# Performance work log

Measured on AMD Instinct MI355X. Metric: run time of the kernel, lower is better.

The kernel has to match this reference:

```python
import jax, jax.numpy as jnp
import numpy as np

BN_EPS = 1e-5

def binary_activation(x):
    # ReActNet BinaryActivation: forward = sign(x), backward = piecewise poly STE
    out_fwd = jnp.sign(x)
    m1 = (x < -1.0).astype(x.dtype)
    m2 = (x < 0.0).astype(x.dtype)
    m3 = (x < 1.0).astype(x.dtype)
    out1 = -1.0 * m1 + (x * x + 2.0 * x) * (1.0 - m1)
    out2 = out1 * m2 + (-x * x + 2.0 * x) * (1.0 - m2)
    out3 = out2 * m3 + 1.0 * (1.0 - m3)
    return jax.lax.stop_gradient(out_fwd - out3) + out3

def binary_conv3x3(x, w, stride=1):
    # per-output-channel scaling = mean |w| over (in, kh, kw), detached
    scale = jax.lax.stop_gradient(jnp.mean(jnp.abs(w), axis=(1, 2, 3), keepdims=True))
    bw_no_grad = jax.lax.stop_gradient(scale * jnp.sign(w))
    cw = jnp.clip(w, -1.0, 1.0)
    bw = bw_no_grad - jax.lax.stop_gradient(cw) + cw
    return jax.lax.conv_general_dilated(
        x, bw, window_strides=(stride, stride), padding=[(1, 1), (1, 1)],
        dimension_numbers=('NCHW', 'OIHW', 'NCHW'))

def batchnorm_inference(y, gamma, beta, mean, var):
    inv = gamma * jax.lax.rsqrt(var + BN_EPS)
    return y * inv[None, :, None, None] + (beta - mean * inv)[None, :, None, None]

def setup_inputs() -> dict:
    key = jax.random.key(0)
    k1, k2, k3 = jax.random.split(key, 3)
    N, Cin, Cout, H, W = 64, 128, 128, 56, 56
    x = jax.random.normal(k1, (N, Cin, H, W), dtype=jnp.float32)
    weight = jax.random.normal(k2, (Cout, Cin, 3, 3), dtype=jnp.float32) * 0.1
    gamma = jnp.ones((Cout,), dtype=jnp.float32)
    beta = jnp.zeros((Cout,), dtype=jnp.float32)
    bn_mean = jnp.zeros((Cout,), dtype=jnp.float32)
    bn_var = jax.random.uniform(k3, (Cout,), dtype=jnp.float32)
    return {"x": x, "weight": weight, "gamma": gamma, "beta": beta,
            "bn_mean": bn_mean, "bn_var": bn_var}

def reference(x, weight, gamma, beta, bn_mean, bn_var):
    residual = x
    out = binary_activation(x)
    out = binary_conv3x3(out, weight, stride=1)
    out = batchnorm_inference(out, gamma, beta, bn_mean, bn_var)
    return out + residual
```

## Files before the change

### kernel.cpp

```cpp
#include <hip/hip_runtime.h>


#define N_   64
#define C_   128
#define H_   56
#define W_   56
#define HW_  (H_*W_)
#define PH_  (H_+2)
#define PW_  (W_+2)
#define PHW_ (PH_*PW_)
#define NPIX (N_*HW_)
#define NPAD (N_*PHW_)

typedef unsigned long long u64;

__global__ void prep_w_kernel(const float* __restrict__ w,
                              const float* __restrict__ gamma,
                              const float* __restrict__ beta,
                              const float* __restrict__ bn_mean,
                              const float* __restrict__ bn_var,
                              u64* __restrict__ wbits,
                              float* __restrict__ A, float* __restrict__ B) {
    const int o = blockIdx.x;
    const int lane = threadIdx.x;
    const float* wo = w + o * 1152;

    float s = 0.f;
    #pragma unroll
    for (int k = 0; k < 18; k++) s += fabsf(wo[k * 64 + lane]);
    #pragma unroll
    for (int off = 32; off > 0; off >>= 1) s += __shfl_down(s, off);
    float scale = __shfl(s, 0) * (1.0f / 1152.0f);

    #pragma unroll
    for (int t = 0; t < 9; t++) {
        #pragma unroll
        for (int j = 0; j < 2; j++) {
            float v = wo[(j * 64 + lane) * 9 + t];
            u64 b = __ballot(v < 0.0f);
            if (lane == 0) wbits[(o * 9 + t) * 2 + j] = b;
        }
    }
    if (lane == 0) {
        float inv = gamma[o] * rsqrtf(bn_var[o] + 1e-5f);
        A[o] = scale * inv;
        B[o] = beta[o] - bn_mean[o] * inv;
    }
}

__global__ __launch_bounds__(256) void pack_x_kernel(
        const float* __restrict__ x,
        ulonglong2* __restrict__ xbs,
        ulonglong2* __restrict__ xbz,
        unsigned* __restrict__ xcnt) {
    int t = blockIdx.x * 256 + threadIdx.x;
    int p = t * 2;
    int n = p / HW_;
    int r = p - n * HW_;
    int h = r / W_;
    int w = r - h * W_;

    const float2* xp = (const float2*)(x + (size_t)n * C_ * HW_ + h * W_ + w);

    unsigned pa[4], za[4], pb[4], zb[4];
    #pragma unroll
    for (int j = 0; j < 4; j++) { pa[j]=0; za[j]=0; pb[j]=0; zb[j]=0; }

    #pragma unroll
    for (int j = 0; j < 4; j++) {
        unsigned paj = 0, zaj = 0, pbj = 0, zbj = 0;
        #pragma unroll 16
        for (int c = 0; c < 32; c++) {
            float2 v = xp[(size_t)(j * 32 + c) * (HW_ / 2)];
            unsigned ua = __float_as_uint(v.x);
            unsigned ub = __float_as_uint(v.y);
            paj |= (ua >> 31) << c;
            zaj |= ((ua << 1) != 0u ? 1u : 0u) << c;
            pbj |= (ub >> 31) << c;
            zbj |= ((ub << 1) != 0u ? 1u : 0u) << c;
        }
        pa[j]=paj; za[j]=zaj; pb[j]=pbj; zb[j]=zbj;
    }

    int pg = (n * PH_ + h + 1) * PW_ + (w + 1);
    ulonglong2 s2, z2;
    s2.x = (u64)pa[0] | ((u64)pa[1] << 32);
    s2.y = (u64)pa[2] | ((u64)pa[3] << 32);
    z2.x = (u64)za[0] | ((u64)za[1] << 32);
    z2.y = (u64)za[2] | ((u64)za[3] << 32);
    xbs[pg] = s2; xbz[pg] = z2;
    xcnt[pg] = __popc(za[0]) + __popc(za[1]) + __popc(za[2]) + __popc(za[3]);

    s2.x = (u64)pb[0] | ((u64)pb[1] << 32);
    s2.y = (u64)pb[2] | ((u64)pb[3] << 32);
    z2.x = (u64)zb[0] | ((u64)zb[1] << 32);
    z2.y = (u64)zb[2] | ((u64)zb[3] << 32);
    xbs[pg + 1] = s2; xbz[pg + 1] = z2;
    xcnt[pg + 1] = __popc(zb[0]) + __popc(zb[1]) + __popc(zb[2]) + __popc(zb[3]);
}

__global__ void border_kernel(ulonglong2* __restrict__ xbs,
                              ulonglong2* __restrict__ xbz,
                              unsigned* __restrict__ xcnt) {
    int bt = blockIdx.x * 256 + threadIdx.x;
    if (bt >= N_ * 228) return;
    int n = bt / 228, e = bt - n * 228;
    int ph, pw;
    if (e < 58)       { ph = 0;  pw = e; }
    else if (e < 116) { ph = 57; pw = e - 58; }
    else { int i = e - 116; ph = 1 + (i >> 1); pw = (i & 1) ? 57 : 0; }
    int g = (n * PH_ + ph) * PW_ + pw;
    ulonglong2 zz; zz.x = 0; zz.y = 0;
    xbs[g] = zz; xbz[g] = zz; xcnt[g] = 0;
}

__device__ __forceinline__ int tapmask_of(int idx) {
    int tm = 0;
    if (idx & 1) tm |= 0x007;
    if (idx & 2) tm |= 0x1C0;
    if (idx & 4) tm |= 0x049;
    if (idx & 8) tm |= 0x124;
    return tm;
}

__global__ __launch_bounds__(256, 6) void bconv_kernel(
        const ulonglong2* __restrict__ xbs,
        const ulonglong2* __restrict__ xbz,
        const unsigned*   __restrict__ xcnt,
        const u64* __restrict__ wbits,
        const float* __restrict__ Ag, const float* __restrict__ Bg,
        const float* __restrict__ x, float* __restrict__ out) {
    __shared__ float2 AB_s[16 * 64];

    const int tid = threadIdx.x;
    const int obase = blockIdx.y * 64;

    for (int e = tid; e < 1024; e += 256) {
        int idx = e >> 6, o = (e & 63);
        int tm = tapmask_of(idx);
        const u64* wp = wbits + (size_t)(obase + o) * 18;
        int s = 0;
        #pragma unroll
        for (int t = 0; t < 9; t++) {
            if ((tm >> t) & 1)
                s += 128 - 2 * (__popcll(wp[2*t]) + __popcll(wp[2*t+1]));
        }
        float a = Ag[obase + o];
        float2 ab; ab.x = a; ab.y = Bg[obase + o] - a * (float)s;
        AB_s[e] = ab;
    }
    __syncthreads();

    int g = blockIdx.x * 256 + tid;
    int n = g / HW_;
    int r = g - n * HW_;
    int h = r / W_;
    int w = r - h * W_;
    int pb = (n * PH_ + h + 1) * PW_ + (w + 1);

    u64 sx[9], sy[9];
    int taps_off[9];
    int csum = 0;
    #pragma unroll
    for (int dh = 0; dh < 3; dh++) {
        #pragma unroll
        for (int dw = 0; dw < 3; dw++) {
            int k = dh * 3 + dw;
            int idx = pb + (dh - 1) * PW_ + (dw - 1);
            taps_off[k] = idx;
            ulonglong2 t2 = xbs[idx];
            sx[k] = t2.x; sy[k] = t2.y;
            csum += (int)xcnt[idx];
        }
    }

    int pidx = (h == 0 ? 1 : 0) | (h == H_-1 ? 2 : 0) |
               (w == 0 ? 4 : 0) | (w == W_-1 ? 8 : 0);
    int valid = 9 - __popc(tapmask_of(pidx));
    bool slow = (csum != 128 * valid);

    const float* xr = x   + ((size_t)n * C_ + obase) * HW_ + r;
    float*       op = out + ((size_t)n * C_ + obase) * HW_ + r;
    const float2* abp = &AB_s[pidx << 6];

    if (!slow) {
        const u64* wp = wbits + (size_t)obase * 18;
        #pragma unroll 2
        for (int o = 0; o < 64; o++) {
            int pc = 0;
            #pragma unroll
            for (int k = 0; k < 9; k++) {
                pc += __popcll(sx[k] ^ wp[2*k]);
                pc += __popcll(sy[k] ^ wp[2*k+1]);
            }
            wp += 18;
            float2 ab = abp[o];
            float dot = (float)(1152 - 2 * pc);
            op[o * HW_] = fmaf(ab.x, dot, ab.y) + xr[o * HW_];
        }
    } else {
        for (int o = 0; o < 64; o++) {
            const u64* wp = wbits + (size_t)(obase + o) * 18;
            int pc = 0;
            #pragma unroll
            for (int k = 0; k < 9; k++) {
                ulonglong2 zz = xbz[taps_off[k]];
                pc += __popcll((sx[k] ^ wp[2*k])   & zz.x);
                pc += __popcll((sy[k] ^ wp[2*k+1]) & zz.y);
            }
            float a = abp[o].x;
            int dot = csum - 2 * pc;
            op[o * HW_] = fmaf(a, (float)dot, Bg[obase + o]) + xr[o * HW_];
        }
    }
}

extern "C" void kernel_launch(void* const* d_in, const int* in_sizes, int n_in,
                              void* d_out, int out_size, void* d_ws, size_t ws_size,
                              hipStream_t stream) {
    const float* x      = (const float*)d_in[0];
    const float* weight = (const float*)d_in[1];
    const float* gamma  = (const float*)d_in[2];
    const float* beta   = (const float*)d_in[3];
    const float* bnmean = (const float*)d_in[4];
    const float* bnvar  = (const float*)d_in[5];
    float* out = (float*)d_out;

    char* ws = (char*)d_ws;
    u64*        wbits = (u64*)ws;
    float*      A     = (float*)(ws + 18432);
    float*      B     = (float*)(ws + 18944);
    ulonglong2* xbs   = (ulonglong2*)(ws + 19456);
    ulonglong2* xbz   = (ulonglong2*)(ws + 19456 + (size_t)NPAD * 16);
    unsigned*   xcnt  = (unsigned*)(ws + 19456 + (size_t)NPAD * 32);

    prep_w_kernel<<<128, 64, 0, stream>>>(weight, gamma, beta, bnmean, bnvar,
                                          wbits, A, B);
    pack_x_kernel<<<NPIX / 2 / 256, 256, 0, stream>>>(x, xbs, xbz, xcnt);
    border_kernel<<<(N_ * 228 + 255) / 256, 256, 0, stream>>>(xbs, xbz, xcnt);
    dim3 cgrid(NPIX / 256, 2);
    bconv_kernel<<<cgrid, 256, 0, stream>>>(xbs, xbz, xcnt, wbits, A, B,
                                            x, out);
}
```

Before: 272.1 us.

## Compute four adjacent pixels per thread with sliding-window tap reuse in binary conv

Each conv thread now handles four horizontally adjacent output pixels. It loads a 3x6 window of packed sign bits once and reuses each weight word across four popcounts, and it reads the residual and writes the output as float4. The output-channel split goes from 64 to 32 per block, the BN/scale constants are folded into one precomputed -2a term plus a per-border bias table, and the pack kernel likewise handles four pixels with float4 loads. This raises register pressure (occupancy hint lowered to 4) and makes the zero-aware slow path apply to a whole group if any one pixel needs it.

Measured after the change: 305.4 us. 12.2% more time.

```diff
diff --git a/kernel.cpp b/kernel.cpp
--- a/kernel.cpp
+++ b/kernel.cpp
@@ -11,6 +11,9 @@
 #define PHW_ (PH_*PW_)
 #define NPIX (N_*HW_)
 #define NPAD (N_*PHW_)
+#define NGRP (NPIX/4)
+#define GPI  (HW_/4)
+#define GPR  (W_/4)
 
 typedef unsigned long long u64;
 
@@ -20,7 +23,8 @@
                               const float* __restrict__ bn_mean,
                               const float* __restrict__ bn_var,
                               u64* __restrict__ wbits,
-                              float* __restrict__ A, float* __restrict__ B) {
+                              float* __restrict__ A, float* __restrict__ B,
+                              float* __restrict__ A2) {
     const int o = blockIdx.x;
     const int lane = threadIdx.x;
     const float* wo = w + o * 1152;
@@ -43,60 +47,60 @@
     }
     if (lane == 0) {
         float inv = gamma[o] * rsqrtf(bn_var[o] + 1e-5f);
-        A[o] = scale * inv;
+        float a = scale * inv;
+        A[o] = a;
         B[o] = beta[o] - bn_mean[o] * inv;
-    }
-}
-
-__global__ __launch_bounds__(256) void pack_x_kernel(
+        A2[o] = -2.0f * a;
+    }
+}
+
+__global__ __launch_bounds__(128) void pack_x_kernel(
         const float* __restrict__ x,
         ulonglong2* __restrict__ xbs,
         ulonglong2* __restrict__ xbz,
         unsigned* __restrict__ xcnt) {
-    int t = blockIdx.x * 256 + threadIdx.x;
-    int p = t * 2;
-    int n = p / HW_;
-    int r = p - n * HW_;
-    int h = r / W_;
-    int w = r - h * W_;
-
-    const float2* xp = (const float2*)(x + (size_t)n * C_ * HW_ + h * W_ + w);
-
-    unsigned pa[4], za[4], pb[4], zb[4];
-    #pragma unroll
-    for (int j = 0; j < 4; j++) { pa[j]=0; za[j]=0; pb[j]=0; zb[j]=0; }
+    int t = blockIdx.x * 128 + threadIdx.x;
+    int n   = t / GPI;
+    int rem = t - n * GPI;
+    int h   = rem / GPR;
+    int wg  = rem - h * GPR;
+    int w   = wg * 4;
+
+    const float4* xp = (const float4*)(x + (size_t)n * C_ * HW_ + h * W_ + w);
+
+    unsigned sg[4][4], nz[4][4];
+    #pragma unroll
+    for (int p = 0; p < 4; p++)
+        #pragma unroll
+        for (int j = 0; j < 4; j++) { sg[p][j] = 0; nz[p][j] = 0; }
 
     #pragma unroll
     for (int j = 0; j < 4; j++) {
-        unsigned paj = 0, zaj = 0, pbj = 0, zbj = 0;
-        #pragma unroll 16
+        #pragma unroll 8
         for (int c = 0; c < 32; c++) {
-            float2 v = xp[(size_t)(j * 32 + c) * (HW_ / 2)];
-            unsigned ua = __float_as_uint(v.x);
-            unsigned ub = __float_as_uint(v.y);
-            paj |= (ua >> 31) << c;
-            zaj |= ((ua << 1) != 0u ? 1u : 0u) << c;
-            pbj |= (ub >> 31) << c;
-            zbj |= ((ub << 1) != 0u ? 1u : 0u) << c;
-        }
-        pa[j]=paj; za[j]=zaj; pb[j]=pbj; zb[j]=zbj;
+            float4 v = xp[(size_t)(j * 32 + c) * (HW_ / 4)];
+            unsigned u0 = __float_as_uint(v.x), u1 = __float_as_uint(v.y);
+            unsigned u2 = __float_as_uint(v.z), u3 = __float_as_uint(v.w);
+            sg[0][j] |= (u0 >> 31) << c; nz[0][j] |= ((u0 << 1) != 0u ? 1u : 0u) << c;
+            sg[1][j] |= (u1 >> 31) << c; nz[1][j] |= ((u1 << 1) != 0u ? 1u : 0u) << c;
+            sg[2][j] |= (u2 >> 31) << c; nz[2][j] |= ((u2 << 1) != 0u ? 1u : 0u) << c;
+            sg[3][j] |= (u3 >> 31) << c; nz[3][j] |= ((u3 << 1) != 0u ? 1u : 0u) << c;
+        }
     }
 
     int pg = (n * PH_ + h + 1) * PW_ + (w + 1);
-    ulonglong2 s2, z2;
-    s2.x = (u64)pa[0] | ((u64)pa[1] << 32);
-    s2.y = (u64)pa[2] | ((u64)pa[3] << 32);
-    z2.x = (u64)za[0] | ((u64)za[1] << 32);
-    z2.y = (u64)za[2] | ((u64)za[3] << 32);
-    xbs[pg] = s2; xbz[pg] = z2;
-    xcnt[pg] = __popc(za[0]) + __popc(za[1]) + __popc(za[2]) + __popc(za[3]);
-
-    s2.x = (u64)pb[0] | ((u64)pb[1] << 32);
-    s2.y = (u64)pb[2] | ((u64)pb[3] << 32);
-    z2.x = (u64)zb[0] | ((u64)zb[1] << 32);
-    z2.y = (u64)zb[2] | ((u64)zb[3] << 32);
-    xbs[pg + 1] = s2; xbz[pg + 1] = z2;
-    xcnt[pg + 1] = __popc(zb[0]) + __popc(zb[1]) + __popc(zb[2]) + __popc(zb[3]);
+    #pragma unroll
+    for (int p = 0; p < 4; p++) {
+        ulonglong2 s2, z2;
+        s2.x = (u64)sg[p][0] | ((u64)sg[p][1] << 32);
+        s2.y = (u64)sg[p][2] | ((u64)sg[p][3] << 32);
+        z2.x = (u64)nz[p][0] | ((u64)nz[p][1] << 32);
+        z2.y = (u64)nz[p][2] | ((u64)nz[p][3] << 32);
+        xbs[pg + p] = s2;
+        xbz[pg + p] = z2;
+        xcnt[pg + p] = __popc(nz[p][0]) + __popc(nz[p][1]) +
+                       __popc(nz[p][2]) + __popc(nz[p][3]);
+    }
 }
 
 __global__ void border_kernel(ulonglong2* __restrict__ xbs,
@@ -123,94 +127,143 @@
     return tm;
 }
 
-__global__ __launch_bounds__(256, 6) void bconv_kernel(
+__global__ __launch_bounds__(256, 4) void bconv_kernel(
         const ulonglong2* __restrict__ xbs,
         const ulonglong2* __restrict__ xbz,
         const unsigned*   __restrict__ xcnt,
         const u64* __restrict__ wbits,
         const float* __restrict__ Ag, const float* __restrict__ Bg,
+        const float* __restrict__ A2g,
         const float* __restrict__ x, float* __restrict__ out) {
-    __shared__ float2 AB_s[16 * 64];
+    __shared__ float Bf_s[16 * 32];
 
     const int tid = threadIdx.x;
-    const int obase = blockIdx.y * 64;
-
-    for (int e = tid; e < 1024; e += 256) {
-        int idx = e >> 6, o = (e & 63);
-        int tm = tapmask_of(idx);
+    const int obase = blockIdx.y * 32;
+
+    for (int e = tid; e < 512; e += 256) {
+        int pidx = e >> 5, o = e & 31;
+        int tm = tapmask_of(pidx);
         const u64* wp = wbits + (size_t)(obase + o) * 18;
         int s = 0;
         #pragma unroll
-        for (int t = 0; t < 9; t++) {
-            if ((tm >> t) & 1)
-                s += 128 - 2 * (__popcll(wp[2*t]) + __popcll(wp[2*t+1]));
+        for (int tp = 0; tp < 9; tp++) {
+            if ((tm >> tp) & 1)
+                s += 128 - 2 * (__popcll(wp[2*tp]) + __popcll(wp[2*tp+1]));
         }
         float a = Ag[obase + o];
-        float2 ab; ab.x = a; ab.y = Bg[obase + o] - a * (float)s;
-        AB_s[e] = ab;
+        Bf_s[e] = fmaf(a, (float)(1152 - s), Bg[obase + o]);
     }
     __syncthreads();
 
-    int g = blockIdx.x * 256 + tid;
-    int n = g / HW_;
-    int r = g - n * HW_;
-    int h = r / W_;
-    int w = r - h * W_;
-    int pb = (n * PH_ + h + 1) * PW_ + (w + 1);
-
-    u64 sx[9], sy[9];
-    int taps_off[9];
-    int csum = 0;
+    int t = blockIdx.x * 256 + tid;
+    int n   = t / GPI;
+    int rem = t - n * GPI;
+    int h   = rem / GPR;
+    int wg  = rem - h * GPR;
+    int w   = wg * 4;
+
+    u64 S0[3][6], S1[3][6];
+    unsigned cnt[3][6];
+    int rowg[3];
     #pragma unroll
     for (int dh = 0; dh < 3; dh++) {
-        #pragma unroll
-        for (int dw = 0; dw < 3; dw++) {
-            int k = dh * 3 + dw;
-            int idx = pb + (dh - 1) * PW_ + (dw - 1);
-            taps_off[k] = idx;
-            ulonglong2 t2 = xbs[idx];
-            sx[k] = t2.x; sy[k] = t2.y;
-            csum += (int)xcnt[idx];
-        }
-    }
-
-    int pidx = (h == 0 ? 1 : 0) | (h == H_-1 ? 2 : 0) |
-               (w == 0 ? 4 : 0) | (w == W_-1 ? 8 : 0);
-    int valid = 9 - __popc(tapmask_of(pidx));
-    bool slow = (csum != 128 * valid);
-
-    const float* xr = x   + ((size_t)n * C_ + obase) * HW_ + r;
-    float*       op = out + ((size_t)n * C_ + obase) * HW_ + r;
-    const float2* abp = &AB_s[pidx << 6];
-
-    if (!slow) {
+        int base = (n * PH_ + h + dh) * PW_ + w;
+        rowg[dh] = base;
+        #pragma unroll
+        for (int j = 0; j < 6; j++) {
+            ulonglong2 v = xbs[base + j];
+            S0[dh][j] = v.x; S1[dh][j] = v.y;
+        }
+        #pragma unroll
+        for (int j = 0; j < 3; j++) {
+            uint2 c2 = *(const uint2*)&xcnt[base + 2*j];
+            cnt[dh][2*j] = c2.x; cnt[dh][2*j+1] = c2.y;
+        }
+    }
+
+    int pidxs[4];
+    bool fastall = true;
+    #pragma unroll
+    for (int p = 0; p < 4; p++) {
+        int ww = w + p;
+        int pidx = (h == 0 ? 1 : 0) | (h == H_-1 ? 2 : 0) |
+                   (ww == 0 ? 4 : 0) | (ww == W_-1 ? 8 : 0);
+        pidxs[p] = pidx;
+        int valid = 9 - __popc(tapmask_of(pidx));
+        int cs = 0;
+        #pragma unroll
+        for (int dh = 0; dh < 3; dh++)
+            cs += cnt[dh][p] + cnt[dh][p+1] + cnt[dh][p+2];
+        fastall = fastall && (cs == 128 * valid);
+    }
+
+    size_t pixoff = (size_t)(n * C_ + obase) * HW_ + h * W_ + w;
+    const float4* xr = (const float4*)(x + pixoff);
+    float4*       op = (float4*)(out + pixoff);
+    const int step4 = HW_ / 4;
+
+    if (fastall) {
         const u64* wp = wbits + (size_t)obase * 18;
-        #pragma unroll 2
-        for (int o = 0; o < 64; o++) {
-            int pc = 0;
+        const float* bf0 = &Bf_s[pidxs[0] << 5];
+        const float* bf1 = &Bf_s[pidxs[1] << 5];
+        const float* bf2 = &Bf_s[pidxs[2] << 5];
+        const float* bf3 = &Bf_s[pidxs[3] << 5];
+        for (int o = 0; o < 32; o++) {
+            int pc0 = 0, pc1 = 0, pc2 = 0, pc3 = 0;
             #pragma unroll
-            for (int k = 0; k < 9; k++) {
-                pc += __popcll(sx[k] ^ wp[2*k]);
-                pc += __popcll(sy[k] ^ wp[2*k+1]);
+            for (int dh = 0; dh < 3; dh++) {
+                #pragma unroll
+                for (int dw = 0; dw < 3; dw++) {
+                    u64 w0 = wp[(dh*3+dw)*2], w1 = wp[(dh*3+dw)*2+1];
+                    pc0 += __popcll(S0[dh][0+dw] ^ w0) + __popcll(S1[dh][0+dw] ^ w1);
+                    pc1 += __popcll(S0[dh][1+dw] ^ w0) + __popcll(S1[dh][1+dw] ^ w1);
+                    pc2 += __popcll(S0[dh][2+dw] ^ w0) + __popcll(S1[dh][2+dw] ^ w1);
+                    pc3 += __popcll(S0[dh][3+dw] ^ w0) + __popcll(S1[dh][3+dw] ^ w1);
+                }
             }
             wp += 18;
-            float2 ab = abp[o];
-            float dot = (float)(1152 - 2 * pc);
-            op[o * HW_] = fmaf(ab.x, dot, ab.y) + xr[o * HW_];
+            float a2 = A2g[obase + o];
+            float4 r = xr[(size_t)o * step4];
+            float4 v;
+            v.x = fmaf(a2, (float)pc0, bf0[o]) + r.x;
+            v.y = fmaf(a2, (float)pc1, bf1[o]) + r.y;
+            v.z = fmaf(a2, (float)pc2, bf2[o]) + r.z;
+            v.w = fmaf(a2, (float)pc3, bf3[o]) + r.w;
+            op[(size_t)o * step4] = v;
         }
     } else {
-        for (int o = 0; o < 64; o++) {
-            const u64* wp = wbits + (size_t)(obase + o) * 18;
-            int pc = 0;
+        #pragma unroll 1
+        for (int p = 0; p < 4; p++) {
+            u64 Z0[3][3], Z1[3][3];
+            int cs = 0;
             #pragma unroll
-            for (int k = 0; k < 9; k++) {
-                ulonglong2 zz = xbz[taps_off[k]];
-                pc += __popcll((sx[k] ^ wp[2*k])   & zz.x);
-                pc += __popcll((sy[k] ^ wp[2*k+1]) & zz.y);
+            for (int dh = 0; dh < 3; dh++) {
+                #pragma unroll
+                for (int dw = 0; dw < 3; dw++) {
+                    int gi = rowg[dh] + p + dw;
+                    ulonglong2 z = xbz[gi];
+                    Z0[dh][dw] = z.x; Z1[dh][dw] = z.y;
+                    cs += (int)xcnt[gi];
+                }
             }
-            float a = abp[o].x;
-            int dot = csum - 2 * pc;
-            op[o * HW_] = fmaf(a, (float)dot, Bg[obase + o]) + xr[o * HW_];
+            const u64* wp = wbits + (size_t)obase * 18;
+            #pragma unroll 1
+            for (int o = 0; o < 32; o++) {
+                int pc = 0;
+                #pragma unroll
+                for (int dh = 0; dh < 3; dh++) {
+                    #pragma unroll
+                    for (int dw = 0; dw < 3; dw++) {
+                        u64 w0 = wp[(dh*3+dw)*2], w1 = wp[(dh*3+dw)*2+1];
+                        pc += __popcll((S0[dh][p+dw] ^ w0) & Z0[dh][dw]);
+                        pc += __popcll((S1[dh][p+dw] ^ w1) & Z1[dh][dw]);
+                    }
+                }
+                wp += 18;
+                float a = Ag[obase + o], b = Bg[obase + o];
+                size_t off = pixoff + (size_t)o * HW_ + p;
+                out[off] = fmaf(a, (float)(cs - 2 * pc), b) + x[off];
+            }
         }
     }
 }
@@ -230,15 +283,16 @@
     u64*        wbits = (u64*)ws;
     float*      A     = (float*)(ws + 18432);
     float*      B     = (float*)(ws + 18944);
-    ulonglong2* xbs   = (ulonglong2*)(ws + 19456);
-    ulonglong2* xbz   = (ulonglong2*)(ws + 19456 + (size_t)NPAD * 16);
-    unsigned*   xcnt  = (unsigned*)(ws + 19456 + (size_t)NPAD * 32);
+    float*      A2    = (float*)(ws + 19456);
+    ulonglong2* xbs   = (ulonglong2*)(ws + 19968);
+    ulonglong2* xbz   = (ulonglong2*)(ws + 19968 + (size_t)NPAD * 16);
+    unsigned*   xcnt  = (unsigned*)(ws + 19968 + (size_t)NPAD * 32);
 
     prep_w_kernel<<<128, 64, 0, stream>>>(weight, gamma, beta, bnmean, bnvar,
-                                          wbits, A, B);
-    pack_x_kernel<<<NPIX / 2 / 256, 256, 0, stream>>>(x, xbs, xbz, xcnt);
+                                          wbits, A, B, A2);
+    pack_x_kernel<<<NGRP / 128, 128, 0, stream>>>(x, xbs, xbz, xcnt);
     border_kernel<<<(N_ * 228 + 255) / 256, 256, 0, stream>>>(xbs, xbz, xcnt);
-    dim3 cgrid(NPIX / 256, 2);
-    bconv_kernel<<<cgrid, 256, 0, stream>>>(xbs, xbz, xcnt, wbits, A, B,
+    dim3 cgrid(NGRP / 256, 4);
+    bconv_kernel<<<cgrid, 256, 0, stream>>>(xbs, xbz, xcnt, wbits, A, B, A2,
                                             x, out);
 }
```
